# Kernel tuning notes

Measured on AMD Instinct MI355X. Metric: run time of the kernel, lower is better.

## Reference

```python
import jax, jax.numpy as jnp
import numpy as np

N_USERS = 50000
N_ENTITIES = 100000
CHANNEL = 64
N_FACTORS = 4
N_REL = 9  # n_relations; weight has N_REL-1 rows
N_EDGES = 1_500_000
NNZ = 800_000
N_HOPS = 2


def _l2_normalize(x, eps=1e-12):
    # matches torch F.normalize(dim=1)
    n = jnp.sqrt(jnp.sum(x * x, axis=1, keepdims=True))
    return x / jnp.maximum(n, eps)


def _distance_correlation(t1, t2):
    # t1, t2: [d] rows of disen_weight_att (d = n_relations-1)
    ch = t1.shape[0]
    t1 = t1[:, None]
    t2 = t2[:, None]
    a_ = (t1 @ t1.T) * 2.0
    b_ = (t2 @ t2.T) * 2.0
    t1s = t1 ** 2
    t2s = t2 ** 2
    a = jnp.sqrt(jnp.maximum(t1s - a_ + t1s.T, 0.0) + 1e-8)
    b = jnp.sqrt(jnp.maximum(t2s - b_ + t2s.T, 0.0) + 1e-8)
    A = a - a.mean(axis=0, keepdims=True) - a.mean(axis=1, keepdims=True) + a.mean()
    B = b - b.mean(axis=0, keepdims=True) - b.mean(axis=1, keepdims=True) + b.mean()
    dcov_AB = jnp.sqrt(jnp.maximum((A * B).sum() / ch ** 2, 0.0) + 1e-8)
    dcov_AA = jnp.sqrt(jnp.maximum((A * A).sum() / ch ** 2, 0.0) + 1e-8)
    dcov_BB = jnp.sqrt(jnp.maximum((B * B).sum() / ch ** 2, 0.0) + 1e-8)
    return dcov_AB / jnp.sqrt(dcov_AA * dcov_BB + 1e-8)


def _cul_cor(disen_weight_att):
    cor = jnp.asarray(0.0, disen_weight_att.dtype)
    for i in range(N_FACTORS):
        for j in range(i + 1, N_FACTORS):
            cor = cor + _distance_correlation(disen_weight_att[i], disen_weight_att[j])
    return cor


def setup_inputs() -> dict:
    key = jax.random.key(0)
    ks = jax.random.split(key, 11)
    return {
        "user_emb": jax.random.normal(ks[0], (N_USERS, CHANNEL), jnp.float32) * 0.1,
        "entity_emb": jax.random.normal(ks[1], (N_ENTITIES, CHANNEL), jnp.float32) * 0.1,
        "latent_emb": jax.random.normal(ks[2], (N_FACTORS, CHANNEL), jnp.float32) * 0.1,
        "weight": jax.random.normal(ks[3], (N_REL - 1, CHANNEL), jnp.float32) * 0.1,
        "disen_weight_att": jax.random.normal(ks[4], (N_FACTORS, N_REL - 1), jnp.float32) * 0.1,
        "interact_vals": jax.random.uniform(ks[5], (NNZ,), jnp.float32),
        "head": jax.random.randint(ks[6], (N_EDGES,), 0, N_ENTITIES),
        "tail": jax.random.randint(ks[7], (N_EDGES,), 0, N_ENTITIES),
        "edge_type": jax.random.randint(ks[8], (N_EDGES,), 1, N_REL),  # in [1, N_REL-1]
        "interact_rows": jax.random.randint(ks[9], (NNZ,), 0, N_USERS),
        "interact_cols": jax.random.randint(ks[10], (NNZ,), 0, N_ENTITIES),
    }


def reference(user_emb, entity_emb, latent_emb, weight, disen_weight_att,
              interact_vals, head, tail, edge_type, interact_rows, interact_cols):
    n_entities = entity_emb.shape[0]
    n_users = user_emb.shape[0]
    cor = _cul_cor(disen_weight_att)

    entity_res = entity_emb
    user_res = user_emb
    ones_e = jnp.ones((head.shape[0],), entity_emb.dtype)
    cnt = jax.ops.segment_sum(ones_e, head, num_segments=n_entities)  # reused: head fixed
    cnt = jnp.maximum(cnt, 1.0)[:, None]

    for _ in range(N_HOPS):
        # KG aggregate: gather tail emb * relation emb, scatter-mean by head
        rel_emb = weight[edge_type - 1]                      # [E, C]
        msg = entity_emb[tail] * rel_emb                     # [E, C]
        entity_agg = jax.ops.segment_sum(msg, head, num_segments=n_entities) / cnt

        # user -> latent factor attention
        score = jax.nn.softmax(user_emb @ latent_emb.T, axis=1)   # [U, F]

        # user aggregate: sparse.mm(interact_mat, entity_emb)
        gathered = interact_vals[:, None] * entity_emb[interact_cols]  # [nnz, C]
        user_agg = jax.ops.segment_sum(gathered, interact_rows, num_segments=n_users)

        disen_weight = jax.nn.softmax(disen_weight_att, axis=-1) @ weight  # [F, C]
        mix = score @ disen_weight                                          # [U, C]
        user_new = user_agg * mix + user_agg

        entity_emb = _l2_normalize(entity_agg)
        user_emb = _l2_normalize(user_new)
        entity_res = entity_res + entity_emb
        user_res = user_res + user_emb

    return entity_res, user_res, cor
```

## Files before the change

kernel.cpp:

```cpp
#include <hip/hip_runtime.h>
#include <math.h>

constexpr int CH         = 64;
constexpr int N_USERS    = 50000;
constexpr int N_ENTITIES = 100000;
constexpr int N_FACTORS  = 4;
constexpr int N_RELM1    = 8;
constexpr int N_EDGES    = 1500000;
constexpr int NNZ        = 800000;

constexpr int NBE        = (N_ENTITIES + 255) / 256;
constexpr int NBU        = (N_USERS + 255) / 256;
constexpr int NBKT       = NBE + NBU;
constexpr int TOTAL      = N_EDGES + NNZ;
constexpr int IPB        = 4096;
constexpr int NBLK       = (TOTAL + IPB - 1) / IPB;
constexpr int CAP_E      = 4352;
constexpr int CAP_U      = 4608;
constexpr int ENT_PAIRS_ = (N_ENTITIES * CH) / 2;
constexpr int NBF16B     = ENT_PAIRS_ / 256;
constexpr int MEGA_BLKS  = NBLK + NBF16B + 2;
constexpr int ENT_BLK8   = N_ENTITIES / 8;
constexpr int USR_BLK8   = N_USERS / 8;

typedef unsigned int u32;
typedef float __attribute__((ext_vector_type(4))) f32x4;

__device__ __forceinline__ u32 pack_bf16x2(float a, float b) {
    u32 ua = __float_as_uint(a), ub = __float_as_uint(b);
    u32 ra = (ua + 0x7FFFu + ((ua >> 16) & 1u)) >> 16;
    u32 rb = (ub + 0x7FFFu + ((ub >> 16) & 1u)) >> 16;
    return ra | (rb << 16);
}
__device__ __forceinline__ float bf_lo(u32 v) { return __uint_as_float(v << 16); }
__device__ __forceinline__ float bf_hi(u32 v) { return __uint_as_float(v & 0xFFFF0000u); }

__device__ __forceinline__ float4 nt_ld4f(const float4* p) {
    f32x4 v = __builtin_nontemporal_load((const f32x4*)p);
    return make_float4(v.x, v.y, v.z, v.w);
}
__device__ __forceinline__ void nt_st4f(float4* p, float4 v) {
    f32x4 t; t.x = v.x; t.y = v.y; t.z = v.z; t.w = v.w;
    __builtin_nontemporal_store(t, (f32x4*)p);
}

__device__ __forceinline__ uint4 gz(const u32* __restrict__ t, int r, int c8, bool v) {
    uint4 x = make_uint4(0u, 0u, 0u, 0u);
    if (v) x = ((const uint4*)t)[r * 8 + c8];
    return x;
}

__global__ __launch_bounds__(256)
void mega_stage(const int* __restrict__ head, const int* __restrict__ tail,
                const int* __restrict__ etype,
                const int* __restrict__ irows, const int* __restrict__ icols,
                const float* __restrict__ ivals,
                int* __restrict__ Bcnt,
                u32* __restrict__ stageE, u32* __restrict__ stageU,
                float* __restrict__ stageUv,
                const float* __restrict__ entity_emb, u32* __restrict__ entB,
                const float* __restrict__ att, const float* __restrict__ weight,
                float* __restrict__ dw, float* __restrict__ cor_out) {
    __shared__ int hist[NBKT];
    __shared__ int cur[NBKT];
    __shared__ float part[6];
    int bid = blockIdx.x;
    if (bid < NBLK) {
        for (int j = threadIdx.x; j < NBKT; j += 256) hist[j] = 0;
        __syncthreads();
        int start = bid * IPB;
        int keys[IPB / 256];
        #pragma unroll
        for (int q = 0; q < IPB / 256; ++q) {
            int i = start + q * 256 + threadIdx.x;
            int k = 0;
            if (i < TOTAL) {
                if (i < N_EDGES) { k = head[i];            atomicAdd(&hist[k >> 8], 1); }
                else             { k = irows[i - N_EDGES]; atomicAdd(&hist[NBE + (k >> 8)], 1); }
            }
            keys[q] = k;
        }
        __syncthreads();
        for (int j = threadIdx.x; j < NBKT; j += 256) {
            int hv = hist[j];
            cur[j] = (hv > 0) ? atomicAdd(&Bcnt[j], hv) : 0;
        }
        __syncthreads();
        #pragma unroll
        for (int q = 0; q < IPB / 256; ++q) {
            int i = start + q * 256 + threadIdx.x;
            if (i >= TOTAL) continue;
            int k = keys[q];
            if (i < N_EDGES) {
                int b   = k >> 8;
                int rel = atomicAdd(&cur[b], 1);
                if (rel < CAP_E)
                    stageE[b * CAP_E + rel] =
                        (u32)tail[i] | ((u32)(etype[i] - 1) << 17) | ((u32)(k & 255) << 20);
            } else {
                int ii  = i - N_EDGES;
                int b   = k >> 8;
                int rel = atomicAdd(&cur[NBE + b], 1);
                if (rel < CAP_U) {
                    stageU[b * CAP_U + rel]  = (u32)icols[ii] | ((u32)(k & 255) << 17);
                    stageUv[b * CAP_U + rel] = ivals[ii];
                }
            }
        }
    } else if (bid < NBLK + NBF16B) {
        int i = (bid - NBLK) * 256 + threadIdx.x;
        float2 f = ((const float2*)entity_emb)[i];
        entB[i] = pack_bf16x2(f.x, f.y);
    } else if (bid == NBLK + NBF16B) {
        int f = threadIdx.x >> 6;
        int c = threadIdx.x & 63;
        float m = -1e30f;
        #pragma unroll
        for (int j = 0; j < N_RELM1; ++j) m = fmaxf(m, att[f * N_RELM1 + j]);
        float s = 0.0f, w[N_RELM1];
        #pragma unroll
        for (int j = 0; j < N_RELM1; ++j) { w[j] = expf(att[f * N_RELM1 + j] - m); s += w[j]; }
        float acc = 0.0f;
        #pragma unroll
        for (int j = 0; j < N_RELM1; ++j) acc += w[j] * weight[j * CH + c];
        dw[f * CH + c] = acc / s;
    } else {
        int w    = threadIdx.x >> 6;
        int lane = threadIdx.x & 63;
        const int pi[6] = {0, 0, 0, 1, 1, 2};
        const int pj[6] = {1, 2, 3, 2, 3, 3};
        int r = lane >> 3, c = lane & 7;
        for (int pp = w; pp < 6; pp += 4) {
            const float* t1 = att + pi[pp] * N_RELM1;
            const float* t2 = att + pj[pp] * N_RELM1;
            float a  = sqrtf(fmaxf(t1[r] * t1[r] - 2.0f * t1[r] * t1[c] + t1[c] * t1[c], 0.0f) + 1e-8f);
            float bb = sqrtf(fmaxf(t2[r] * t2[r] - 2.0f * t2[r] * t2[c] + t2[c] * t2[c], 0.0f) + 1e-8f);
            float rsA = a, rsB = bb;
            #pragma unroll
            for (int o = 1; o < 8; o <<= 1) { rsA += __shfl_xor(rsA, o, 64); rsB += __shfl_xor(rsB, o, 64); }
            float csA = a, csB = bb;
            #pragma unroll
            for (int o = 8; o < 64; o <<= 1) { csA += __shfl_xor(csA, o, 64); csB += __shfl_xor(csB, o, 64); }
            float totA = rsA, totB = rsB;
            #pragma unroll
            for (int o = 8; o < 64; o <<= 1) { totA += __shfl_xor(totA, o, 64); totB += __shfl_xor(totB, o, 64); }
            float A = a  - csA * 0.125f - rsA * 0.125f + totA * (1.0f / 64.0f);
            float B = bb - csB * 0.125f - rsB * 0.125f + totB * (1.0f / 64.0f);
            float sAB = A * B, sAA = A * A, sBB = B * B;
            #pragma unroll
            for (int o = 1; o < 64; o <<= 1) {
                sAB += __shfl_xor(sAB, o, 64);
                sAA += __shfl_xor(sAA, o, 64);
                sBB += __shfl_xor(sBB, o, 64);
            }
            if (lane == 0) {
                float dAB = sqrtf(fmaxf(sAB * (1.0f / 64.0f), 0.0f) + 1e-8f);
                float dAA = sqrtf(fmaxf(sAA * (1.0f / 64.0f), 0.0f) + 1e-8f);
                float dBB = sqrtf(fmaxf(sBB * (1.0f / 64.0f), 0.0f) + 1e-8f);
                part[pp] = dAB / sqrtf(dAA * dBB + 1e-8f);
            }
        }
        __syncthreads();
        if (threadIdx.x == 0) {
            float s = 0.0f;
            for (int q = 0; q < 6; ++q) s += part[q];
            cor_out[0] = s;
        }
    }
}

__global__ __launch_bounds__(256)
void bin_fill3(const int* __restrict__ Bcnt,
               const u32* __restrict__ stageE, const u32* __restrict__ stageU,
               const float* __restrict__ stageUv,
               int* __restrict__ offE, int* __restrict__ offU,
               int* __restrict__ elst, int* __restrict__ ucol,
               float* __restrict__ uval) {
    __shared__ int khist[256];
    __shared__ int cur[256];
    __shared__ int wsum[4];
    int b = blockIdx.x, t = threadIdx.x;
    int w = t >> 6, lane = t & 63;
    bool isE = (b < NBE);
    int seg0 = isE ? 0 : NBE;
    int cap  = isE ? CAP_E : CAP_U;
    int partial = 0;
    for (int i = seg0 + t; i < b; i += 256) partial += min(Bcnt[i], cap);
    #pragma unroll
    for (int o = 1; o < 64; o <<= 1) partial += __shfl_xor(partial, o, 64);
    if (lane == 0) wsum[w] = partial;
    __syncthreads();
    int gbase = wsum[0] + wsum[1] + wsum[2] + wsum[3];
    __syncthreads();
    khist[t] = 0;
    __syncthreads();
    if (isE) {
        int n = min(Bcnt[b], CAP_E);
        const u32* src = stageE + b * CAP_E;
        for (int i = t; i < n; i += 256)
            atomicAdd(&khist[(src[i] >> 20) & 255], 1);
        __syncthreads();
        int v = khist[t];
        int incl = v;
        #pragma unroll
        for (int d = 1; d < 64; d <<= 1) {
            int u = __shfl_up(incl, d, 64);
            if (lane >= d) incl += u;
        }
        if (lane == 63) wsum[w] = incl;
        __syncthreads();
        int base = 0;
        #pragma unroll
        for (int q = 0; q < 4; ++q) if (q < w) base += wsum[q];
        int excl = base + incl - v;
        int key  = b * 256 + t;
        if (key < N_ENTITIES) offE[key] = gbase + excl;
        cur[t] = gbase + excl;
        if (b == 0 && t == 0) offE[N_ENTITIES] = N_EDGES;
        __syncthreads();
        for (int i = t; i < n; i += 256) {
            u32 s = src[i];
            int p = atomicAdd(&cur[(s >> 20) & 255], 1);
            elst[p] = (int)(s & 0xFFFFFu);
        }
    } else {
        int bu = b - NBE;
        int n = min(Bcnt[b], CAP_U);
        const u32*   src  = stageU  + bu * CAP_U;
        const float* srcv = stageUv + bu * CAP_U;
        for (int i = t; i < n; i += 256)
            atomicAdd(&khist[(src[i] >> 17) & 255], 1);
        __syncthreads();
        int v = khist[t];
        int incl = v;
        #pragma unroll
        for (int d = 1; d < 64; d <<= 1) {
            int u = __shfl_up(incl, d, 64);
            if (lane >= d) incl += u;
        }
        if (lane == 63) wsum[w] = incl;
        __syncthreads();
        int base = 0;
        #pragma unroll
        for (int q = 0; q < 4; ++q) if (q < w) base += wsum[q];
        int excl = base + incl - v;
        int key  = bu * 256 + t;
        if (key < N_USERS) offU[key] = gbase + excl;
        cur[t] = gbase + excl;
        if (b == NBE && t == 0) offU[N_USERS] = NNZ;
        __syncthreads();
        for (int i = t; i < n; i += 256) {
            u32 s = src[i];
            float vv = srcv[i];
            int p = atomicAdd(&cur[(s >> 17) & 255], 1);
            ucol[p] = (int)(s & 0x1FFFFu);
            uval[p] = vv;
        }
    }
}

__device__ __forceinline__ void acc_edge(float* acc, uint4 xv, float4 wa, float4 wb) {
    acc[0] += bf_lo(xv.x) * wa.x; acc[1] += bf_hi(xv.x) * wa.y;
    acc[2] += bf_lo(xv.y) * wa.z; acc[3] += bf_hi(xv.y) * wa.w;
    acc[4] += bf_lo(xv.z) * wb.x; acc[5] += bf_hi(xv.z) * wb.y;
    acc[6] += bf_lo(xv.w) * wb.z; acc[7] += bf_hi(xv.w) * wb.w;
}
__device__ __forceinline__ void acc_user(float* acc, uint4 xv, float vv) {
    acc[0] += vv * bf_lo(xv.x); acc[1] += vv * bf_hi(xv.x);
    acc[2] += vv * bf_lo(xv.y); acc[3] += vv * bf_hi(xv.y);
    acc[4] += vv * bf_lo(xv.z); acc[5] += vv * bf_hi(xv.z);
    acc[6] += vv * bf_lo(xv.w); acc[7] += vv * bf_hi(xv.w);
}

template <bool HOP0>
__global__ __launch_bounds__(256)
void hop_pass(const u32* __restrict__ entB,
              const float* __restrict__ usr_in,
              const float* __restrict__ weight, const float* __restrict__ latent,
              const float* __restrict__ dw,
              const int* __restrict__ offE, const int* __restrict__ elst,
              const int* __restrict__ offU, const int* __restrict__ ucol,
              const float* __restrict__ uval,
              u32* __restrict__ AeB_out,
              float* __restrict__ Au_out,
              float* __restrict__ ent_res, float* __restrict__ usr_res,
              const float* __restrict__ ent_base, const float* __restrict__ usr_base) {
    __shared__ float4 w4[N_RELM1 * 16];
    int lane = threadIdx.x & 63;
    int h    = lane >> 5;
    int g    = (lane >> 3) & 3;
    int c8   = lane & 7;
    int l5   = lane & 31;
    float acc[8] = {0.f, 0.f, 0.f, 0.f, 0.f, 0.f, 0.f, 0.f};

    if ((int)blockIdx.x < ENT_BLK8) {
        if (threadIdx.x < N_RELM1 * 16)
            w4[threadIdx.x] = ((const float4*)weight)[threadIdx.x];
        __syncthreads();
        int row = blockIdx.x * 8 + ((threadIdx.x >> 6) << 1) + h;
        int lo = offE[row], hi = offE[row + 1];
        for (int k0 = lo; k0 < hi; k0 += 32) {
            int m = min(32, hi - k0);
            int p = elst[min(k0 + l5, N_EDGES - 1)];
            for (int jj = 0; jj < m; jj += 16) {
                int j0 = jj + g;
                int q0 = __shfl(p, j0,      32);
                int q1 = __shfl(p, j0 + 4,  32);
                int q2 = __shfl(p, j0 + 8,  32);
                int q3 = __shfl(p, j0 + 12, 32);
                uint4 x0 = gz(entB, q0 & 0x1FFFF, c8, j0      < m);
                uint4 x1 = gz(entB, q1 & 0x1FFFF, c8, j0 + 4  < m);
                uint4 x2 = gz(entB, q2 & 0x1FFFF, c8, j0 + 8  < m);
                uint4 x3 = gz(entB, q3 & 0x1FFFF, c8, j0 + 12 < m);
                float4 wa0 = w4[(q0 >> 17) * 16 + (c8 << 1)];
                float4 wb0 = w4[(q0 >> 17) * 16 + (c8 << 1) + 1];
                float4 wa1 = w4[(q1 >> 17) * 16 + (c8 << 1)];
                float4 wb1 = w4[(q1 >> 17) * 16 + (c8 << 1) + 1];
                float4 wa2 = w4[(q2 >> 17) * 16 + (c8 << 1)];
                float4 wb2 = w4[(q2 >> 17) * 16 + (c8 << 1) + 1];
                float4 wa3 = w4[(q3 >> 17) * 16 + (c8 << 1)];
                float4 wb3 = w4[(q3 >> 17) * 16 + (c8 << 1) + 1];
                acc_edge(acc, x0, wa0, wb0);
                acc_edge(acc, x1, wa1, wb1);
                acc_edge(acc, x2, wa2, wb2);
                acc_edge(acc, x3, wa3, wb3);
            }
        }
        #pragma unroll
        for (int j = 0; j < 8; ++j) {
            acc[j] += __shfl_xor(acc[j], 8, 64);
            acc[j] += __shfl_xor(acc[j], 16, 64);
        }
        float s = 0.0f;
        #pragma unroll
        for (int j = 0; j < 8; ++j) s += acc[j] * acc[j];
        s += __shfl_xor(s, 1, 64);
        s += __shfl_xor(s, 2, 64);
        s += __shfl_xor(s, 4, 64);
        float inv = 1.0f / fmaxf(sqrtf(s), 1e-12f);
        if (g == 0) {
            float y0 = acc[0] * inv, y1 = acc[1] * inv, y2 = acc[2] * inv, y3 = acc[3] * inv;
            float y4 = acc[4] * inv, y5 = acc[5] * inv, y6 = acc[6] * inv, y7 = acc[7] * inv;
            int qi = row * 16 + (c8 << 1);
            if (HOP0) {
                uint4 pk;
                pk.x = pack_bf16x2(y0, y1); pk.y = pack_bf16x2(y2, y3);
                pk.z = pack_bf16x2(y4, y5); pk.w = pack_bf16x2(y6, y7);
                ((uint4*)AeB_out)[row * 8 + c8] = pk;
                float4 b0 = nt_ld4f(&((const float4*)ent_base)[qi]);
                float4 b1 = nt_ld4f(&((const float4*)ent_base)[qi + 1]);
                nt_st4f(&((float4*)ent_res)[qi],     make_float4(b0.x + y0, b0.y + y1, b0.z + y2, b0.w + y3));
                nt_st4f(&((float4*)ent_res)[qi + 1], make_float4(b1.x + y4, b1.y + y5, b1.z + y6, b1.w + y7));
            } else {
                float4 r0 = nt_ld4f(&((const float4*)ent_res)[qi]);
                float4 r1 = nt_ld4f(&((const float4*)ent_res)[qi + 1]);
                nt_st4f(&((float4*)ent_res)[qi],     make_float4(r0.x + y0, r0.y + y1, r0.z + y2, r0.w + y3));
                nt_st4f(&((float4*)ent_res)[qi + 1], make_float4(r1.x + y4, r1.y + y5, r1.z + y6, r1.w + y7));
            }
        }
    } else {
        int row = (blockIdx.x - ENT_BLK8) * 8 + ((threadIdx.x >> 6) << 1) + h;
        int qi  = row * 16 + (c8 << 1);
        float4 u0 = nt_ld4f(&((const float4*)usr_in)[qi]);
        float4 u1 = nt_ld4f(&((const float4*)usr_in)[qi + 1]);
        int lo = offU[row], hi = offU[row + 1];
        for (int k0 = lo; k0 < hi; k0 += 32) {
            int m = min(32, hi - k0);
            int sidx = min(k0 + l5, NNZ - 1);
            int   cl = ucol[sidx];
            float vl = uval[sidx];
            for (int jj = 0; jj < m; jj += 16) {
                int j0 = jj + g;
                int   c0 = __shfl(cl, j0,      32);
                int   c1 = __shfl(cl, j0 + 4,  32);
                int   c2 = __shfl(cl, j0 + 8,  32);
                int   c3 = __shfl(cl, j0 + 12, 32);
                float v0 = __shfl(vl, j0,      32);
                float v1 = __shfl(vl, j0 + 4,  32);
                float v2 = __shfl(vl, j0 + 8,  32);
                float v3 = __shfl(vl, j0 + 12, 32);
                uint4 x0 = gz(entB, c0, c8, j0      < m);
                uint4 x1 = gz(entB, c1, c8, j0 + 4  < m);
                uint4 x2 = gz(entB, c2, c8, j0 + 8  < m);
                uint4 x3 = gz(entB, c3, c8, j0 + 12 < m);
                acc_user(acc, x0, v0);
                acc_user(acc, x1, v1);
                acc_user(acc, x2, v2);
                acc_user(acc, x3, v3);
            }
        }
        #pragma unroll
        for (int j = 0; j < 8; ++j) {
            acc[j] += __shfl_xor(acc[j], 8, 64);
            acc[j] += __shfl_xor(acc[j], 16, 64);
        }
        float d[N_FACTORS];
        #pragma unroll
        for (int f = 0; f < N_FACTORS; ++f) {
            float4 l0 = ((const float4*)latent)[f * 16 + (c8 << 1)];
            float4 l1 = ((const float4*)latent)[f * 16 + (c8 << 1) + 1];
            d[f] = u0.x * l0.x + u0.y * l0.y + u0.z * l0.z + u0.w * l0.w
                 + u1.x * l1.x + u1.y * l1.y + u1.z * l1.z + u1.w * l1.w;
            d[f] += __shfl_xor(d[f], 1, 64);
            d[f] += __shfl_xor(d[f], 2, 64);
            d[f] += __shfl_xor(d[f], 4, 64);
        }
        float mx = fmaxf(fmaxf(d[0], d[1]), fmaxf(d[2], d[3]));
        float ex0 = expf(d[0] - mx), ex1 = expf(d[1] - mx);
        float ex2 = expf(d[2] - mx), ex3 = expf(d[3] - mx);
        float sinv = 1.0f / (ex0 + ex1 + ex2 + ex3);
        float mix[8] = {0.f, 0.f, 0.f, 0.f, 0.f, 0.f, 0.f, 0.f};
        {
            float exf[N_FACTORS] = {ex0, ex1, ex2, ex3};
            #pragma unroll
            for (int f = 0; f < N_FACTORS; ++f) {
                float4 w0 = ((const float4*)dw)[f * 16 + (c8 << 1)];
                float4 w1 = ((const float4*)dw)[f * 16 + (c8 << 1) + 1];
                float ef = exf[f];
                mix[0] += ef * w0.x; mix[1] += ef * w0.y;
                mix[2] += ef * w0.z; mix[3] += ef * w0.w;
                mix[4] += ef * w1.x; mix[5] += ef * w1.y;
                mix[6] += ef * w1.z; mix[7] += ef * w1.w;
            }
            #pragma unroll
            for (int j = 0; j < 8; ++j) mix[j] *= sinv;
        }
        float un[8];
        #pragma unroll
        for (int j = 0; j < 8; ++j) un[j] = acc[j] * (1.0f + mix[j]);
        float s = 0.0f;
        #pragma unroll
        for (int j = 0; j < 8; ++j) s += un[j] * un[j];
        s += __shfl_xor(s, 1, 64);
        s += __shfl_xor(s, 2, 64);
        s += __shfl_xor(s, 4, 64);
        float inv = 1.0f / fmaxf(sqrtf(s), 1e-12f);
        if (g == 0) {
            float y0 = un[0] * inv, y1 = un[1] * inv, y2 = un[2] * inv, y3 = un[3] * inv;
            float y4 = un[4] * inv, y5 = un[5] * inv, y6 = un[6] * inv, y7 = un[7] * inv;
            if (HOP0) {
                nt_st4f(&((float4*)Au_out)[qi],     make_float4(y0, y1, y2, y3));
                nt_st4f(&((float4*)Au_out)[qi + 1], make_float4(y4, y5, y6, y7));
            } else {
                float4 b0 = nt_ld4f(&((const float4*)usr_base)[qi]);
                float4 b1 = nt_ld4f(&((const float4*)usr_base)[qi + 1]);
                nt_st4f(&((float4*)usr_res)[qi],
                        make_float4((b0.x + u0.x) + y0, (b0.y + u0.y) + y1,
                                    (b0.z + u0.z) + y2, (b0.w + u0.w) + y3));
                nt_st4f(&((float4*)usr_res)[qi + 1],
                        make_float4((b1.x + u1.x) + y4, (b1.y + u1.y) + y5,
                                    (b1.z + u1.z) + y6, (b1.w + u1.w) + y7));
            }
        }
    }
}

extern "C" void kernel_launch(void* const* d_in, const int* in_sizes, int n_in,
                              void* d_out, int out_size, void* d_ws, size_t ws_size,
                              hipStream_t stream) {
    const float* user_emb   = (const float*)d_in[0];
    const float* entity_emb = (const float*)d_in[1];
    const float* latent     = (const float*)d_in[2];
    const float* weight     = (const float*)d_in[3];
    const float* att        = (const float*)d_in[4];
    const float* ivals      = (const float*)d_in[5];
    const int*   head       = (const int*)d_in[6];
    const int*   tail       = (const int*)d_in[7];
    const int*   etype      = (const int*)d_in[8];
    const int*   irows      = (const int*)d_in[9];
    const int*   icols      = (const int*)d_in[10];

    float* out     = (float*)d_out;
    float* ent_res = out;
    float* usr_res = out + (size_t)N_ENTITIES * CH;
    float* cor_out = out + (size_t)N_ENTITIES * CH + (size_t)N_USERS * CH;

    const size_t ENT_ELEMS = (size_t)N_ENTITIES * CH;
    const size_t USR_ELEMS = (size_t)N_USERS * CH;
    const int    ENT_PAIRS = (int)(ENT_ELEMS / 2);

    float* ws   = (float*)d_ws;
    u32*   entB = (u32*)ws;
    u32*   AeB  = entB + ENT_PAIRS;
    float* Au   = (float*)(AeB + ENT_PAIRS);
    float* dw   = Au + USR_ELEMS;
    int*   offE = (int*)(dw + N_FACTORS * CH);
    int*   offU = offE + N_ENTITIES + 1;
    int*   elst = offU + N_USERS + 1;
    int*   ucol = elst + N_EDGES;
    float* uval = (float*)(ucol + NNZ);
    u32*   stageE  = AeB;
    u32*   stageU  = stageE + (size_t)NBE * CAP_E;
    float* stageUv = (float*)(stageU + (size_t)NBU * CAP_U);
    int*   Bcnt = (int*)(Au + 1000000);

    hipMemsetAsync(Bcnt, 0, (size_t)NBKT * sizeof(int), stream);
    mega_stage<<<MEGA_BLKS, 256, 0, stream>>>(head, tail, etype, irows, icols, ivals,
                                              Bcnt, stageE, stageU, stageUv,
                                              entity_emb, entB,
                                              att, weight, dw, cor_out);
    bin_fill3<<<NBKT, 256, 0, stream>>>(Bcnt, stageE, stageU, stageUv,
                                        offE, offU, elst, ucol, uval);

    hop_pass<true><<<ENT_BLK8 + USR_BLK8, 256, 0, stream>>>(
        entB, user_emb, weight, latent, dw,
        offE, elst, offU, ucol, uval,
        AeB, Au, ent_res, usr_res, entity_emb, user_emb);

    hop_pass<false><<<ENT_BLK8 + USR_BLK8, 256, 0, stream>>>(
        AeB, Au, weight, latent, dw,
        offE, elst, offU, ucol, uval,
        nullptr, nullptr, ent_res, usr_res, entity_emb, user_emb);
}
```

Baseline: 333.6 us.

## Double items per binning block, reload keys instead of caching, add nontemporal loads

Doubles the number of edges and interactions each binning block handles, which halves the block count and the per-block histogram overhead. The keys are no longer held in registers between the histogram pass and the scatter pass; head and irows are read again from global memory in the second pass. Single-use streams (tail, etype, icols, ivals, the embedding conversion source, staged values) now use nontemporal loads to limit cache pollution. In exchange there are fewer blocks to spread across CUs, more serial work per block, and the key arrays are read twice.

Measured after the change: 346.5 us. 1.04x slower.

```diff
diff --git a/kernel.cpp b/kernel.cpp
--- a/kernel.cpp
+++ b/kernel.cpp
@@ -13,7 +13,7 @@
 constexpr int NBU        = (N_USERS + 255) / 256;
 constexpr int NBKT       = NBE + NBU;
 constexpr int TOTAL      = N_EDGES + NNZ;
-constexpr int IPB        = 4096;
+constexpr int IPB        = 8192;
 constexpr int NBLK       = (TOTAL + IPB - 1) / IPB;
 constexpr int CAP_E      = 4352;
 constexpr int CAP_U      = 4608;
@@ -42,6 +42,13 @@
 __device__ __forceinline__ void nt_st4f(float4* p, float4 v) {
     f32x4 t; t.x = v.x; t.y = v.y; t.z = v.z; t.w = v.w;
     __builtin_nontemporal_store(t, (f32x4*)p);
+}
+__device__ __forceinline__ int    nt_ldi(const int* p)    { return __builtin_nontemporal_load(p); }
+__device__ __forceinline__ float  nt_ldf(const float* p)  { return __builtin_nontemporal_load(p); }
+__device__ __forceinline__ float2 nt_ld2f(const float2* p) {
+    typedef float __attribute__((ext_vector_type(2))) f32x2;
+    f32x2 v = __builtin_nontemporal_load((const f32x2*)p);
+    return make_float2(v.x, v.y);
 }
 
 __device__ __forceinline__ uint4 gz(const u32* __restrict__ t, int r, int c8, bool v) {
@@ -69,16 +76,12 @@
         for (int j = threadIdx.x; j < NBKT; j += 256) hist[j] = 0;
         __syncthreads();
         int start = bid * IPB;
-        int keys[IPB / 256];
-        #pragma unroll
         for (int q = 0; q < IPB / 256; ++q) {
             int i = start + q * 256 + threadIdx.x;
-            int k = 0;
             if (i < TOTAL) {
-                if (i < N_EDGES) { k = head[i];            atomicAdd(&hist[k >> 8], 1); }
-                else             { k = irows[i - N_EDGES]; atomicAdd(&hist[NBE + (k >> 8)], 1); }
-            }
-            keys[q] = k;
+                if (i < N_EDGES) atomicAdd(&hist[head[i] >> 8], 1);
+                else             atomicAdd(&hist[NBE + (irows[i - N_EDGES] >> 8)], 1);
+            }
         }
         __syncthreads();
         for (int j = threadIdx.x; j < NBKT; j += 256) {
@@ -86,30 +89,31 @@
             cur[j] = (hv > 0) ? atomicAdd(&Bcnt[j], hv) : 0;
         }
         __syncthreads();
-        #pragma unroll
         for (int q = 0; q < IPB / 256; ++q) {
             int i = start + q * 256 + threadIdx.x;
             if (i >= TOTAL) continue;
-            int k = keys[q];
             if (i < N_EDGES) {
+                int k   = head[i];
                 int b   = k >> 8;
                 int rel = atomicAdd(&cur[b], 1);
                 if (rel < CAP_E)
                     stageE[b * CAP_E + rel] =
-                        (u32)tail[i] | ((u32)(etype[i] - 1) << 17) | ((u32)(k & 255) << 20);
+                        (u32)nt_ldi(&tail[i]) | ((u32)(nt_ldi(&etype[i]) - 1) << 17)
+                        | ((u32)(k & 255) << 20);
             } else {
                 int ii  = i - N_EDGES;
+                int k   = irows[ii];
                 int b   = k >> 8;
                 int rel = atomicAdd(&cur[NBE + b], 1);
                 if (rel < CAP_U) {
-                    stageU[b * CAP_U + rel]  = (u32)icols[ii] | ((u32)(k & 255) << 17);
-                    stageUv[b * CAP_U + rel] = ivals[ii];
+                    stageU[b * CAP_U + rel]  = (u32)nt_ldi(&icols[ii]) | ((u32)(k & 255) << 17);
+                    stageUv[b * CAP_U + rel] = nt_ldf(&ivals[ii]);
                 }
             }
         }
     } else if (bid < NBLK + NBF16B) {
         int i = (bid - NBLK) * 256 + threadIdx.x;
-        float2 f = ((const float2*)entity_emb)[i];
+        float2 f = nt_ld2f(&((const float2*)entity_emb)[i]);
         entB[i] = pack_bf16x2(f.x, f.y);
     } else if (bid == NBLK + NBF16B) {
         int f = threadIdx.x >> 6;
@@ -251,7 +255,7 @@
         __syncthreads();
         for (int i = t; i < n; i += 256) {
             u32 s = src[i];
-            float vv = srcv[i];
+            float vv = nt_ldf(&srcv[i]);
             int p = atomicAdd(&cur[(s >> 17) & 255], 1);
             ucol[p] = (int)(s & 0x1FFFFu);
             uval[p] = vv;
```
